# Kernel tuning notes

Hardware: AMD Instinct MI355X
Metric: run time of the kernel (lower is better)

## Reference

```python
import jax, jax.numpy as jnp
import numpy as np

B, N, C = 2, 2048, 768
H = 12
D = C // H
SCALE = D ** -0.5
EPS = 1e-5
HID = 4 * C


def layer_norm(x, g, b):
    mu = jnp.mean(x, axis=-1, keepdims=True)
    var = jnp.var(x, axis=-1, keepdims=True)
    return (x - mu) * jax.lax.rsqrt(var + EPS) * g + b


def setup_inputs():
    key = jax.random.key(0)
    ks = jax.random.split(key, 12)
    s = C ** -0.5
    x = jax.random.normal(ks[0], (B, N, C), dtype=jnp.float32)
    mask = (jax.random.uniform(ks[1], (B, N, N)) < 0.1).astype(jnp.float32)
    return {
        "x": x,
        "mask": mask,
        "g1": jnp.ones((C,), jnp.float32),
        "b1": jnp.zeros((C,), jnp.float32),
        "Wq": jax.random.normal(ks[2], (C, C), jnp.float32) * s,
        "Wkv": jax.random.normal(ks[3], (2 * C, C), jnp.float32) * s,
        "Wp": jax.random.normal(ks[4], (C, C), jnp.float32) * s,
        "bp": jnp.zeros((C,), jnp.float32),
        "g2": jnp.ones((C,), jnp.float32),
        "b2": jnp.zeros((C,), jnp.float32),
        "W1": jax.random.normal(ks[5], (HID, C), jnp.float32) * s,
        "bf1": jnp.zeros((HID,), jnp.float32),
        "W2": jax.random.normal(ks[6], (C, HID), jnp.float32) * (HID ** -0.5),
        "bf2": jnpmp if False else jnp.zeros((C,), jnp.float32),
    }


def block_fwd(x, mask, g1, b1, Wq, Wkv, Wp, bp, g2, b2, W1, bf1, W2, bf2):
    # --- attention branch (pre-norm) ---
    xn = layer_norm(x, g1, b1)
    q = (xn @ Wq.T).reshape(B, N, H, D).transpose(0, 2, 1, 3)      # bhnd
    kv = (xn @ Wkv.T).reshape(B, N, 2, H, D).transpose(2, 0, 3, 1, 4)
    k, v = kv[0], kv[1]                                             # bhnd
    attn = jnp.einsum('bhnd,bhmd->bhnm', q, k) * SCALE
    attn = attn + (mask * -100000.0)[:, None]                       # additive mask
    attn = jax.nn.softmax(attn, axis=-1)
    o = jnp.einsum('bhnm,bhmd->bhnd', attn, v)
    o = o.transpose(0, 2, 1, 3).reshape(B, N, C)
    o = o @ Wp.T + bp
    x = x + o
    # --- MLP branch (pre-norm) ---
    xn2 = layer_norm(x, g2, b2)
    h = jax.nn.gelu(xn2 @ W1.T + bf1, approximate=False)
    x = x + (h @ W2.T + bf2)
    return x


def reference(x, mask, g1, b1, Wq, Wkv, Wp, bp, g2, b2, W1, bf1, W2, bf2):
    return block_fwd(x, mask, g1, b1, Wq, Wkv, Wp, bp, g2, b2, W1, bf1, W2, bf2)
```

## Files before the change

kernel.cpp:

```cpp
#include <hip/hip_runtime.h>
#include <hip/hip_bf16.h>
#include <cstdint>
#include <cstddef>

#define BB 2
#define NN 2048
#define CC 768
#define HH 12
#define DD 64
#define HID 3072
#define TT (BB*NN)

typedef __attribute__((ext_vector_type(8))) short bf16x8;
typedef __attribute__((ext_vector_type(4))) short bf16x4;
typedef __attribute__((ext_vector_type(4))) float f32x4;

__device__ __forceinline__ unsigned short f2bf(float f) {
    unsigned int u = __float_as_uint(f);
    u += 0x7fffu + ((u >> 16) & 1u);
    return (unsigned short)(u >> 16);
}
__device__ __forceinline__ float bf2f(unsigned short u) {
    return __uint_as_float(((unsigned int)u) << 16);
}
#if __has_builtin(__builtin_amdgcn_exp2f)
#define EXP2F(x) __builtin_amdgcn_exp2f(x)
#else
#define EXP2F(x) exp2f(x)
#endif

__device__ __forceinline__ void gload16(const void* g, void* l) {
    __builtin_amdgcn_global_load_lds((__attribute__((address_space(1))) unsigned int*)g,
                                     (__attribute__((address_space(3))) unsigned int*)l,
                                     16, 0, 0);
}

#define WAITV(N) asm volatile("s_waitcnt vmcnt(" #N ")" ::: "memory")
#define WAITLGKM asm volatile("s_waitcnt lgkmcnt(0)" ::: "memory")

struct CvtArgs {
    const float* in[5];
    unsigned short* out[5];
    int n4[5];
};
typedef __attribute__((ext_vector_type(4))) float float4v;
typedef __attribute__((ext_vector_type(4))) unsigned short ushort4v;
__global__ __launch_bounds__(256) void cvt5_kernel(CvtArgs a) {
    int base = blockIdx.x * 256 + threadIdx.x;
    int stride = gridDim.x * 256;
#pragma unroll
    for (int s = 0; s < 5; ++s) {
        const float4v* ip = (const float4v*)a.in[s];
        ushort4v* op = (ushort4v*)a.out[s];
        for (int i = base; i < a.n4[s]; i += stride) {
            float4v v = ip[i];
            ushort4v o;
            o[0] = f2bf(v[0]); o[1] = f2bf(v[1]); o[2] = f2bf(v[2]); o[3] = f2bf(v[3]);
            op[i] = o;
        }
    }
}

__global__ __launch_bounds__(256) void maskbits_kernel(const float* __restrict__ mask,
                                                       unsigned short* __restrict__ mb, int n) {
    int i = blockIdx.x * 256 + threadIdx.x;
    if (i >= n) return;
    const float4v* mp = (const float4v*)(mask + (size_t)i * 16);
    unsigned int bits = 0;
#pragma unroll
    for (int q = 0; q < 4; ++q) {
        float4v v = mp[q];
#pragma unroll
        for (int j = 0; j < 4; ++j) bits |= (v[j] > 0.5f) ? (1u << (q * 4 + j)) : 0u;
    }
    mb[i] = (unsigned short)bits;
}

__global__ __launch_bounds__(256) void ln_kernel(const float* __restrict__ x,
                                                 const float* __restrict__ g,
                                                 const float* __restrict__ b,
                                                 unsigned short* __restrict__ out) {
    int t = blockIdx.x;
    int tid = threadIdx.x;
    const float* xr = x + (size_t)t * CC;
    float v0 = xr[tid], v1 = xr[tid + 256], v2 = xr[tid + 512];
    float s = v0 + v1 + v2;
    float s2 = v0 * v0 + v1 * v1 + v2 * v2;
#pragma unroll
    for (int off = 1; off < 64; off <<= 1) {
        s  += __shfl_xor(s, off);
        s2 += __shfl_xor(s2, off);
    }
    __shared__ float red[8];
    int wv = tid >> 6, lane = tid & 63;
    if (lane == 0) { red[wv] = s; red[wv + 4] = s2; }
    __syncthreads();
    s  = red[0] + red[1] + red[2] + red[3];
    s2 = red[4] + red[5] + red[6] + red[7];
    float mu   = s * (1.0f / CC);
    float var  = s2 * (1.0f / CC) - mu * mu;
    float rstd = rsqrtf(var + 1e-5f);
    unsigned short* orow = out + (size_t)t * CC;
    orow[tid]       = f2bf((v0 - mu) * rstd * g[tid]       + b[tid]);
    orow[tid + 256] = f2bf((v1 - mu) * rstd * g[tid + 256] + b[tid + 256]);
    orow[tid + 512] = f2bf((v2 - mu) * rstd * g[tid + 512] + b[tid + 512]);
}

template <int EPI, int BM>
__global__ __launch_bounds__(256) void gemm_bt(const unsigned short* __restrict__ A,
                                               const unsigned short* __restrict__ Bw,
                                               const float* __restrict__ bias,
                                               const float* __restrict__ res,
                                               void* __restrict__ out,
                                               int M, int N, int K) {
    constexpr int MI = BM / 32;
    constexpr int NCA = (BM * 4) / 256;
    __shared__ alignas(16) unsigned short As[2][BM * 32];
    __shared__ alignas(16) unsigned short Bs[2][128 * 32];
    int tid = threadIdx.x;
    int lane = tid & 63, wv = tid >> 6;
    int l16 = lane & 15, lg = lane >> 4;
    int bm = blockIdx.x, bn = blockIdx.y;
    int wm = (wv & 1) * (BM / 2), wn = (wv >> 1) * 64;

    const unsigned short* Ab = A + (size_t)bm * BM * K;
    const unsigned short* Bb = Bw + (size_t)bn * 128 * K;

    const unsigned short* aSrc[NCA]; int aDst[NCA];
#pragma unroll
    for (int i = 0; i < NCA; ++i) {
        int c = tid + i * 256;
        int row = c >> 2, p = c & 3;
        int lc = p ^ ((row >> 1) & 3);
        aSrc[i] = Ab + (size_t)row * K + lc * 8;
        aDst[i] = c * 8;
    }
    const unsigned short* bSrc[2]; int bDst[2];
#pragma unroll
    for (int i = 0; i < 2; ++i) {
        int c = tid + i * 256;
        int row = c >> 2, p = c & 3;
        int lc = p ^ ((row >> 1) & 3);
        bSrc[i] = Bb + (size_t)row * K + lc * 8;
        bDst[i] = c * 8;
    }
    int aoff = (wm + l16) * 32 + ((lg ^ (((wm + l16) >> 1) & 3)) * 8);
    int boff = (wn + l16) * 32 + ((lg ^ (((wn + l16) >> 1) & 3)) * 8);

    f32x4 acc[MI][4];
#pragma unroll
    for (int i = 0; i < MI; ++i)
#pragma unroll
        for (int j = 0; j < 4; ++j) acc[i][j] = f32x4{0.f, 0.f, 0.f, 0.f};

    auto STAGE = [&](int s, int k0) {
#pragma unroll
        for (int i = 0; i < NCA; ++i) gload16(aSrc[i] + k0, &As[s][aDst[i]]);
#pragma unroll
        for (int i = 0; i < 2; ++i)   gload16(bSrc[i] + k0, &Bs[s][bDst[i]]);
    };

    STAGE(0, 0);
    int nt = K / 32;
    for (int t = 0; t < nt; ++t) {
        int cur = t & 1;
        if (t + 1 < nt) {
            STAGE(cur ^ 1, (t + 1) * 32);
            if constexpr (NCA + 2 == 4) { WAITV(4); } else { WAITV(3); }
        } else {
            WAITV(0);
        }
        __builtin_amdgcn_s_barrier();
        bf16x8 af[MI], bfr[4];
#pragma unroll
        for (int mi = 0; mi < MI; ++mi) af[mi]  = *(const bf16x8*)&As[cur][aoff + mi * 512];
#pragma unroll
        for (int ni = 0; ni < 4; ++ni)  bfr[ni] = *(const bf16x8*)&Bs[cur][boff + ni * 512];
#pragma unroll
        for (int mi = 0; mi < MI; ++mi)
#pragma unroll
            for (int ni = 0; ni < 4; ++ni)
                acc[mi][ni] = __builtin_amdgcn_mfma_f32_16x16x32_bf16(bfr[ni], af[mi], acc[mi][ni], 0, 0, 0);
        WAITLGKM;
        __builtin_amdgcn_s_barrier();
    }

#pragma unroll
    for (int mi = 0; mi < MI; ++mi) {
        int row = bm * BM + wm + mi * 16 + l16;
#pragma unroll
        for (int ni = 0; ni < 4; ++ni) {
            int col = bn * 128 + wn + ni * 16 + lg * 4;
            size_t idx = (size_t)row * N + col;
            f32x4 v = acc[mi][ni];
            if (EPI == 0) {
                bf16x4 ov;
#pragma unroll
                for (int r = 0; r < 4; ++r) ov[r] = (short)f2bf(v[r]);
                *(bf16x4*)((unsigned short*)out + idx) = ov;
            } else if (EPI == 1 || EPI == 3) {
                f32x4 bv = *(const f32x4*)&bias[col];
                f32x4 rv = *(const f32x4*)&res[idx];
                f32x4 ov;
#pragma unroll
                for (int r = 0; r < 4; ++r) ov[r] = v[r] + bv[r] + rv[r];
                *(f32x4*)((float*)out + idx) = ov;
            } else {
                f32x4 bv = *(const f32x4*)&bias[col];
                bf16x4 ov;
#pragma unroll
                for (int r = 0; r < 4; ++r) {
                    float t2 = v[r] + bv[r];
                    t2 = 0.5f * t2 * (1.0f + erff(t2 * 0.70710678118f));
                    ov[r] = (short)f2bf(t2);
                }
                *(bf16x4*)((unsigned short*)out + idx) = ov;
            }
        }
    }
}

#define KVB 64
#define ANT (NN/KVB)
#define VP 68
__global__ __launch_bounds__(256, 4) void attn_kernel(const unsigned short* __restrict__ qkv,
                                                      const unsigned short* __restrict__ maskb,
                                                      unsigned short* __restrict__ o) {
    __shared__ alignas(16) unsigned short Ks[2][64 * 64];
    __shared__ alignas(16) unsigned short Vt[2][64 * VP];
    int tid = threadIdx.x;
    int lane = tid & 63, wv = tid >> 6;
    int l16 = lane & 15, lg = lane >> 4;
    int qb = blockIdx.x;
    int bh = blockIdx.y;
    int b = bh / HH, h = bh % HH;
    int qrow = qb * 64 + wv * 16 + l16;

    const unsigned short* qp = qkv + ((size_t)(b * NN + qrow)) * 2304 + h * DD;
    bf16x8 q0r = *(const bf16x8*)(qp + 8 * lg);
    bf16x8 q1r = *(const bf16x8*)(qp + 32 + 8 * lg);
    const float QSC = 0.125f * 1.4426950408889634f;
    bf16x8 q0, q1;
#pragma unroll
    for (int j = 0; j < 8; ++j) {
        q0[j] = (short)f2bf(bf2f((unsigned short)q0r[j]) * QSC);
        q1[j] = (short)f2bf(bf2f((unsigned short)q1r[j]) * QSC);
    }

    const unsigned short* mrow  = maskb + ((size_t)(b * NN + qrow)) * 128;
    const unsigned short* kbase = qkv + (size_t)b * NN * 2304 + 768 + h * DD;
    const unsigned short* vbase = qkv + (size_t)b * NN * 2304 + 1536 + h * DD;

    const unsigned short* kSrc[2]; int kDst[2];
#pragma unroll
    for (int i = 0; i < 2; ++i) {
        int c = tid + i * 256;
        int row = c >> 3, p = c & 7;
        int lc = p ^ (row & 7);
        kSrc[i] = kbase + (size_t)row * 2304 + lc * 8;
        kDst[i] = c * 8;
    }
    int kp = tid & 31, dg = tid >> 5;
    const unsigned short* vSrc = vbase + (size_t)(2 * kp) * 2304 + dg * 8;

    int sw = l16 & 7;
    int kb0 = l16 * 64 + ((lg ^ sw) * 8);
    int kb1 = l16 * 64 + (((lg + 4) ^ sw) * 8);
    int vbo = l16 * VP + lg * 4;

    bf16x8 va, vb;
    unsigned long long mb_cur, mb_nxt;

    f32x4 oa[4];
#pragma unroll
    for (int i = 0; i < 4; ++i) oa[i] = f32x4{0.f, 0.f, 0.f, 0.f};
    float mrun = -INFINITY, lrun = 0.f;

    auto LOAD = [&](int t, int s) {
#pragma unroll
        for (int i = 0; i < 2; ++i) gload16(kSrc[i] + (size_t)t * KVB * 2304, &Ks[s][kDst[i]]);
        const unsigned short* vp = vSrc + (size_t)t * KVB * 2304;
        va = *(const bf16x8*)(vp);
        vb = *(const bf16x8*)(vp + 2304);
        mb_nxt = *(const unsigned long long*)(mrow + t * 4);
    };
    auto WRITEV = [&](int s) {
        unsigned int* VtU = (unsigned int*)Vt[s];
#pragma unroll
        for (int j = 0; j < 8; ++j)
            VtU[(dg * 8 + j) * (VP / 2) + kp] =
                (unsigned int)(unsigned short)va[j] | ((unsigned int)(unsigned short)vb[j] << 16);
    };

    LOAD(0, 0);
    WRITEV(0);
    mb_cur = mb_nxt;
    __syncthreads();
    int cur = 0;

    for (int kt = 0; kt < ANT; ++kt) {
        bool pre = (kt + 1 < ANT);
        if (pre) LOAD(kt + 1, cur ^ 1);
        const unsigned short* Ksc = Ks[cur];
        const unsigned short* Vtc = Vt[cur];

        float sv[16];
#pragma unroll
        for (int ks = 0; ks < 4; ++ks) {
            bf16x8 k0 = *(const bf16x8*)&Ksc[kb0 + ks * 1024];
            bf16x8 k1 = *(const bf16x8*)&Ksc[kb1 + ks * 1024];
            f32x4 sa = f32x4{0.f, 0.f, 0.f, 0.f};
            sa = __builtin_amdgcn_mfma_f32_16x16x32_bf16(k0, q0, sa, 0, 0, 0);
            sa = __builtin_amdgcn_mfma_f32_16x16x32_bf16(k1, q1, sa, 0, 0, 0);
            unsigned int m16 = (unsigned int)(mb_cur >> (ks * 16 + lg * 4));
#pragma unroll
            for (int r = 0; r < 4; ++r) {
                float mbit = (float)((m16 >> r) & 1u);
                sv[ks * 4 + r] = fmaf(mbit, -144269.5f, sa[r]);
            }
        }
        float tmax = sv[0];
#pragma unroll
        for (int i = 1; i < 16; ++i) tmax = fmaxf(tmax, sv[i]);
        tmax = fmaxf(tmax, __shfl_xor(tmax, 16));
        tmax = fmaxf(tmax, __shfl_xor(tmax, 32));

        if (__any(tmax > mrun + 11.5f)) {
            float mnew = fmaxf(mrun, tmax);
            float sc = EXP2F(mrun - mnew);
            lrun *= sc;
#pragma unroll
            for (int db = 0; db < 4; ++db) {
                oa[db][0] *= sc; oa[db][1] *= sc; oa[db][2] *= sc; oa[db][3] *= sc;
            }
            mrun = mnew;
        }

        float ps = 0.f;
        bf16x4 pf[4];
#pragma unroll
        for (int ks = 0; ks < 4; ++ks)
#pragma unroll
            for (int r = 0; r < 4; ++r) {
                float p = EXP2F(sv[ks * 4 + r] - mrun);
                ps += p;
                pf[ks][r] = (short)f2bf(p);
            }
        lrun += ps;

#pragma unroll
        for (int ks = 0; ks < 4; ++ks)
#pragma unroll
            for (int db = 0; db < 4; ++db) {
                bf16x4 vf = *(const bf16x4*)&Vtc[vbo + db * 16 * VP + ks * 16];
                oa[db] = __builtin_amdgcn_mfma_f32_16x16x16bf16_1k(vf, pf[ks], oa[db], 0, 0, 0);
            }

        if (pre) WRITEV(cur ^ 1);
        __syncthreads();
        if (pre) { cur ^= 1; mb_cur = mb_nxt; }
    }

    float lt = lrun;
    lt += __shfl_xor(lt, 16);
    lt += __shfl_xor(lt, 32);
    float inv = 1.0f / lt;
    unsigned short* op = o + ((size_t)(b * NN + qrow)) * CC + h * DD;
#pragma unroll
    for (int db = 0; db < 4; ++db) {
        bf16x4 ov;
#pragma unroll
        for (int r = 0; r < 4; ++r) ov[r] = (short)f2bf(oa[db][r] * inv);
        *(bf16x4*)&op[db * 16 + lg * 4] = ov;
    }
}

extern "C" void kernel_launch(void* const* d_in, const int* in_sizes, int n_in,
                              void* d_out, int out_size, void* d_ws, size_t ws_size,
                              hipStream_t stream) {
    const float* x    = (const float*)d_in[0];
    const float* mask = (const float*)d_in[1];
    const float* g1   = (const float*)d_in[2];
    const float* b1   = (const float*)d_in[3];
    const float* Wq   = (const float*)d_in[4];
    const float* Wkv  = (const float*)d_in[5];
    const float* Wp   = (const float*)d_in[6];
    const float* bp   = (const float*)d_in[7];
    const float* g2   = (const float*)d_in[8];
    const float* b2   = (const float*)d_in[9];
    const float* W1   = (const float*)d_in[10];
    const float* bf1  = (const float*)d_in[11];
    const float* W2   = (const float*)d_in[12];
    const float* bf2  = (const float*)d_in[13];
    float* out = (float*)d_out;

    char* w = (char*)d_ws;
    unsigned short* wqkv = (unsigned short*)w;      w += (size_t)2304 * 768 * 2;
    unsigned short* wp   = (unsigned short*)w;      w += (size_t)768 * 768 * 2;
    unsigned short* w1   = (unsigned short*)w;      w += (size_t)3072 * 768 * 2;
    unsigned short* w2   = (unsigned short*)w;      w += (size_t)768 * 3072 * 2;
    unsigned short* xn   = (unsigned short*)w;      w += (size_t)TT * CC * 2;
    unsigned short* qkv  = (unsigned short*)w;      w += (size_t)TT * 2304 * 2;
    unsigned short* mb   = (unsigned short*)w;      w += (size_t)BB * NN * 128 * 2;
    unsigned short* obuf = (unsigned short*)w;      w += (size_t)TT * CC * 2;
    float*          x1   = (float*)w;               w += (size_t)TT * CC * 4;
    unsigned short* xn2  = (unsigned short*)w;      w += (size_t)TT * CC * 2;
    unsigned short* hbuf = (unsigned short*)w;      w += (size_t)TT * HID * 2;

    CvtArgs ca;
    ca.in[0] = Wq;  ca.out[0] = wqkv;             ca.n4[0] = 768 * 768 / 4;
    ca.in[1] = Wkv; ca.out[1] = wqkv + 768 * 768; ca.n4[1] = 1536 * 768 / 4;
    ca.in[2] = Wp;  ca.out[2] = wp;               ca.n4[2] = 768 * 768 / 4;
    ca.in[3] = W1;  ca.out[3] = w1;               ca.n4[3] = 3072 * 768 / 4;
    ca.in[4] = W2;  ca.out[4] = w2;               ca.n4[4] = 768 * 3072 / 4;
    cvt5_kernel<<<1024, 256, 0, stream>>>(ca);

    {
        int n = BB * NN * (NN / 16);
        maskbits_kernel<<<(n + 255) / 256, 256, 0, stream>>>(mask, mb, n);
    }

    ln_kernel<<<TT, 256, 0, stream>>>(x, g1, b1, xn);

    gemm_bt<0, 128><<<dim3(TT / 128, 2304 / 128), 256, 0, stream>>>(xn, wqkv, nullptr, nullptr, qkv, TT, 2304, 768);

    attn_kernel<<<dim3(NN / 64, BB * HH), 256, 0, stream>>>(qkv, mb, obuf);

    gemm_bt<1, 64><<<dim3(TT / 64, 768 / 128), 256, 0, stream>>>(obuf, wp, bp, x, x1, TT, 768, 768);

    ln_kernel<<<TT, 256, 0, stream>>>(x1, g2, b2, xn2);

    gemm_bt<2, 128><<<dim3(TT / 128, HID / 128), 256, 0, stream>>>(xn2, w1, bf1, nullptr, hbuf, TT, HID, 768);

    gemm_bt<3, 64><<<dim3(TT / 64, 768 / 128), 256, 0, stream>>>(hbuf, w2, bf2, x1, out, TT, 768, HID);
}
```

Baseline: 219.9 us.

## Fuse prep kernels, remap attention blocks per XCD, truncate P to bf16

Merges the weight conversion, mask bit-packing and first layernorm into one prep kernel, removing two launches and letting the three pieces of work overlap. The attention grid becomes 1D, with each XCD given a fixed set of three (batch, head) pairs so K/V reuse stays inside one L2. The attention launch-bounds occupancy hint is dropped. Softmax probabilities are now truncated to bf16 instead of rounded, trading a little accuracy for fewer ALU ops.

```diff
diff --git a/kernel.cpp b/kernel.cpp
--- a/kernel.cpp
+++ b/kernel.cpp
@@ -38,42 +38,70 @@
 #define WAITV(N) asm volatile("s_waitcnt vmcnt(" #N ")" ::: "memory")
 #define WAITLGKM asm volatile("s_waitcnt lgkmcnt(0)" ::: "memory")
 
-struct CvtArgs {
-    const float* in[5];
-    unsigned short* out[5];
-    int n4[5];
-};
 typedef __attribute__((ext_vector_type(4))) float float4v;
 typedef __attribute__((ext_vector_type(4))) unsigned short ushort4v;
-__global__ __launch_bounds__(256) void cvt5_kernel(CvtArgs a) {
-    int base = blockIdx.x * 256 + threadIdx.x;
-    int stride = gridDim.x * 256;
-#pragma unroll
-    for (int s = 0; s < 5; ++s) {
-        const float4v* ip = (const float4v*)a.in[s];
-        ushort4v* op = (ushort4v*)a.out[s];
-        for (int i = base; i < a.n4[s]; i += stride) {
-            float4v v = ip[i];
-            ushort4v o;
-            o[0] = f2bf(v[0]); o[1] = f2bf(v[1]); o[2] = f2bf(v[2]); o[3] = f2bf(v[3]);
-            op[i] = o;
-        }
-    }
-}
-
-__global__ __launch_bounds__(256) void maskbits_kernel(const float* __restrict__ mask,
-                                                       unsigned short* __restrict__ mb, int n) {
-    int i = blockIdx.x * 256 + threadIdx.x;
-    if (i >= n) return;
-    const float4v* mp = (const float4v*)(mask + (size_t)i * 16);
-    unsigned int bits = 0;
-#pragma unroll
-    for (int q = 0; q < 4; ++q) {
-        float4v v = mp[q];
-#pragma unroll
-        for (int j = 0; j < 4; ++j) bits |= (v[j] > 0.5f) ? (1u << (q * 4 + j)) : 0u;
-    }
-    mb[i] = (unsigned short)bits;
+
+struct PrepArgs {
+    const float* x; const float* g1; const float* b1; unsigned short* xn;
+    const float* cin[5]; unsigned short* cout[5]; int n4[5];
+    const float* mask; unsigned short* mb;
+};
+__global__ __launch_bounds__(256) void prep_kernel(PrepArgs a) {
+    int id = blockIdx.x;
+    int tid = threadIdx.x;
+    if (id < TT) {
+        const float* xr = a.x + (size_t)id * CC;
+        float v0 = xr[tid], v1 = xr[tid + 256], v2 = xr[tid + 512];
+        float s = v0 + v1 + v2;
+        float s2 = v0 * v0 + v1 * v1 + v2 * v2;
+#pragma unroll
+        for (int off = 1; off < 64; off <<= 1) {
+            s  += __shfl_xor(s, off);
+            s2 += __shfl_xor(s2, off);
+        }
+        __shared__ float red[8];
+        int wv = tid >> 6, lane = tid & 63;
+        if (lane == 0) { red[wv] = s; red[wv + 4] = s2; }
+        __syncthreads();
+        s  = red[0] + red[1] + red[2] + red[3];
+        s2 = red[4] + red[5] + red[6] + red[7];
+        float mu   = s * (1.0f / CC);
+        float var  = s2 * (1.0f / CC) - mu * mu;
+        float rstd = rsqrtf(var + 1e-5f);
+        unsigned short* orow = a.xn + (size_t)id * CC;
+        orow[tid]       = f2bf((v0 - mu) * rstd * a.g1[tid]       + a.b1[tid]);
+        orow[tid + 256] = f2bf((v1 - mu) * rstd * a.g1[tid + 256] + a.b1[tid + 256]);
+        orow[tid + 512] = f2bf((v2 - mu) * rstd * a.g1[tid + 512] + a.b1[tid + 512]);
+    } else if (id < TT + 1024) {
+        int base = (id - TT) * 256 + tid;
+        int stride = 1024 * 256;
+#pragma unroll
+        for (int sseg = 0; sseg < 5; ++sseg) {
+            const float4v* ip = (const float4v*)a.cin[sseg];
+            ushort4v* op = (ushort4v*)a.cout[sseg];
+            for (int i = base; i < a.n4[sseg]; i += stride) {
+                float4v v = ip[i];
+                ushort4v o;
+                o[0] = f2bf(v[0]); o[1] = f2bf(v[1]); o[2] = f2bf(v[2]); o[3] = f2bf(v[3]);
+                op[i] = o;
+            }
+        }
+    } else {
+        int base = (id - TT - 1024) * 256 + tid;
+        int stride = 1024 * 256;
+        int n = BB * NN * (NN / 16);
+        for (int i = base; i < n; i += stride) {
+            const float4v* mp = (const float4v*)(a.mask + (size_t)i * 16);
+            unsigned int bits = 0;
+#pragma unroll
+            for (int q = 0; q < 4; ++q) {
+                float4v v = mp[q];
+#pragma unroll
+                for (int j = 0; j < 4; ++j) bits |= (v[j] > 0.5f) ? (1u << (q * 4 + j)) : 0u;
+            }
+            a.mb[i] = (unsigned short)bits;
+        }
+    }
 }
 
 __global__ __launch_bounds__(256) void ln_kernel(const float* __restrict__ x,
@@ -196,23 +224,23 @@
             if (EPI == 0) {
                 bf16x4 ov;
 #pragma unroll
-                for (int r = 0; r < 4; ++r) ov[r] = (short)f2bf(v[r]);
+                for (int r2 = 0; r2 < 4; ++r2) ov[r2] = (short)f2bf(v[r2]);
                 *(bf16x4*)((unsigned short*)out + idx) = ov;
             } else if (EPI == 1 || EPI == 3) {
                 f32x4 bv = *(const f32x4*)&bias[col];
                 f32x4 rv = *(const f32x4*)&res[idx];
                 f32x4 ov;
 #pragma unroll
-                for (int r = 0; r < 4; ++r) ov[r] = v[r] + bv[r] + rv[r];
+                for (int r2 = 0; r2 < 4; ++r2) ov[r2] = v[r2] + bv[r2] + rv[r2];
                 *(f32x4*)((float*)out + idx) = ov;
             } else {
                 f32x4 bv = *(const f32x4*)&bias[col];
                 bf16x4 ov;
 #pragma unroll
-                for (int r = 0; r < 4; ++r) {
-                    float t2 = v[r] + bv[r];
+                for (int r2 = 0; r2 < 4; ++r2) {
+                    float t2 = v[r2] + bv[r2];
                     t2 = 0.5f * t2 * (1.0f + erff(t2 * 0.70710678118f));
-                    ov[r] = (short)f2bf(t2);
+                    ov[r2] = (short)f2bf(t2);
                 }
                 *(bf16x4*)((unsigned short*)out + idx) = ov;
             }
@@ -223,16 +251,18 @@
 #define KVB 64
 #define ANT (NN/KVB)
 #define VP 68
-__global__ __launch_bounds__(256, 4) void attn_kernel(const unsigned short* __restrict__ qkv,
-                                                      const unsigned short* __restrict__ maskb,
-                                                      unsigned short* __restrict__ o) {
+__global__ __launch_bounds__(256) void attn_kernel(const unsigned short* __restrict__ qkv,
+                                                   const unsigned short* __restrict__ maskb,
+                                                   unsigned short* __restrict__ o) {
     __shared__ alignas(16) unsigned short Ks[2][64 * 64];
     __shared__ alignas(16) unsigned short Vt[2][64 * VP];
     int tid = threadIdx.x;
     int lane = tid & 63, wv = tid >> 6;
     int l16 = lane & 15, lg = lane >> 4;
-    int qb = blockIdx.x;
-    int bh = blockIdx.y;
+    int id = blockIdx.x;
+    int xcd = id & 7, r = id >> 3;
+    int bh = xcd * 3 + (r % 3);
+    int qb = r / 3;
     int b = bh / HH, h = bh % HH;
     int qrow = qb * 64 + wv * 16 + l16;
 
@@ -314,9 +344,9 @@
             sa = __builtin_amdgcn_mfma_f32_16x16x32_bf16(k1, q1, sa, 0, 0, 0);
             unsigned int m16 = (unsigned int)(mb_cur >> (ks * 16 + lg * 4));
 #pragma unroll
-            for (int r = 0; r < 4; ++r) {
-                float mbit = (float)((m16 >> r) & 1u);
-                sv[ks * 4 + r] = fmaf(mbit, -144269.5f, sa[r]);
+            for (int r2 = 0; r2 < 4; ++r2) {
+                float mbit = (float)((m16 >> r2) & 1u);
+                sv[ks * 4 + r2] = fmaf(mbit, -144269.5f, sa[r2]);
             }
         }
         float tmax = sv[0];
@@ -341,10 +371,10 @@
 #pragma unroll
         for (int ks = 0; ks < 4; ++ks)
 #pragma unroll
-            for (int r = 0; r < 4; ++r) {
-                float p = EXP2F(sv[ks * 4 + r] - mrun);
+            for (int r2 = 0; r2 < 4; ++r2) {
+                float p = EXP2F(sv[ks * 4 + r2] - mrun);
                 ps += p;
-                pf[ks][r] = (short)f2bf(p);
+                pf[ks][r2] = (short)(__float_as_uint(p) >> 16);
             }
         lrun += ps;
 
@@ -370,7 +400,7 @@
     for (int db = 0; db < 4; ++db) {
         bf16x4 ov;
 #pragma unroll
-        for (int r = 0; r < 4; ++r) ov[r] = (short)f2bf(oa[db][r] * inv);
+        for (int r2 = 0; r2 < 4; ++r2) ov[r2] = (short)f2bf(oa[db][r2] * inv);
         *(bf16x4*)&op[db * 16 + lg * 4] = ov;
     }
 }
@@ -407,24 +437,19 @@
     unsigned short* xn2  = (unsigned short*)w;      w += (size_t)TT * CC * 2;
     unsigned short* hbuf = (unsigned short*)w;      w += (size_t)TT * HID * 2;
 
-    CvtArgs ca;
-    ca.in[0] = Wq;  ca.out[0] = wqkv;             ca.n4[0] = 768 * 768 / 4;
-    ca.in[1] = Wkv; ca.out[1] = wqkv + 768 * 768; ca.n4[1] = 1536 * 768 / 4;
-    ca.in[2] = Wp;  ca.out[2] = wp;               ca.n4[2] = 768 * 768 / 4;
-    ca.in[3] = W1;  ca.out[3] = w1;               ca.n4[3] = 3072 * 768 / 4;
-    ca.in[4] = W2;  ca.out[4] = w2;               ca.n4[4] = 768 * 3072 / 4;
-    cvt5_kernel<<<1024, 256, 0, stream>>>(ca);
-
-    {
-        int n = BB * NN * (NN / 16);
-        maskbits_kernel<<<(n + 255) / 256, 256, 0, stream>>>(mask, mb, n);
-    }
-
-    ln_kernel<<<TT, 256, 0, stream>>>(x, g1, b1, xn);
+    PrepArgs pa;
+    pa.x = x; pa.g1 = g1; pa.b1 = b1; pa.xn = xn;
+    pa.cin[0] = Wq;  pa.cout[0] = wqkv;             pa.n4[0] = 768 * 768 / 4;
+    pa.cin[1] = Wkv; pa.cout[1] = wqkv + 768 * 768; pa.n4[1] = 1536 * 768 / 4;
+    pa.cin[2] = Wp;  pa.cout[2] = wp;               pa.n4[2] = 768 * 768 / 4;
+    pa.cin[3] = W1;  pa.cout[3] = w1;               pa.n4[3] = 3072 * 768 / 4;
+    pa.cin[4] = W2;  pa.cout[4] = w2;               pa.n4[4] = 768 * 3072 / 4;
+    pa.mask = mask; pa.mb = mb;
+    prep_kernel<<<TT + 2048, 256, 0, stream>>>(pa);
 
     gemm_bt<0, 128><<<dim3(TT / 128, 2304 / 128), 256, 0, stream>>>(xn, wqkv, nullptr, nullptr, qkv, TT, 2304, 768);
 
-    attn_kernel<<<dim3(NN / 64, BB * HH), 256, 0, stream>>>(qkv, mb, obuf);
+    attn_kernel<<<32 * 24, 256, 0, stream>>>(qkv, mb, obuf);
 
     gemm_bt<1, 64><<<dim3(TT / 64, 768 / 128), 256, 0, stream>>>(obuf, wp, bp, x, x1, TT, 768, 768);
 
```

New measurement: 216.7 us. No clear change (-1.5%).
